# Optimization experiments

Hardware: AMD Instinct MI355X
Metric: run time of the kernel (lower is better)

The kernel has to match this reference:

```python
import jax, jax.numpy as jnp
import numpy as np

# Reconstructed GTS forecasting module (DCGRU encoder-decoder, eval mode / no teacher forcing).
N = 5000        # nodes_num
U = 32          # rnn_units
IN = 1          # node_features per step
K = 2           # max_diffusion_step -> supports [X, A@X, A@A@X]
T_ENC = 12
T_DEC = 12
DIN = (K + 1) * (IN + U)


def setup_inputs() -> dict:
    key = jax.random.key(0)
    ks = jax.random.split(key, 12)
    def p(k, shape, scale=0.1):
        return jax.random.normal(k, shape, dtype=jnp.float32) * scale
    inputs = jax.random.normal(ks[0], (N, T_ENC), dtype=jnp.float32)
    targets = jax.random.normal(ks[1], (N, T_DEC), dtype=jnp.float32)
    adj = jax.random.uniform(ks[2], (N, N), dtype=jnp.float32)
    adj = adj / jnp.sum(adj, axis=1, keepdims=True)  # random-walk normalized support
    return {
        'inputs': inputs, 'targets': targets, 'adj_matrix': adj,
        'enc_Wg': p(ks[3], (DIN, 2 * U)), 'enc_bg': jnp.zeros((2 * U,), jnp.float32),
        'enc_Wc': p(ks[4], (DIN, U)),     'enc_bc': jnp.zeros((U,), jnp.float32),
        'dec_Wg': p(ks[5], (DIN, 2 * U)), 'dec_bg': jnp.zeros((2 * U,), jnp.float32),
        'dec_Wc': p(ks[6], (DIN, U)),     'dec_bc': jnp.zeros((U,), jnp.float32),
        'dec_Wp': p(ks[7], (U, 1)),       'dec_bp': jnp.zeros((1,), jnp.float32),
    }


def _gconv(x, h, adj, W, b):
    # diffusion graph convolution over supports [I, A, A^2]
    xh = jnp.concatenate([x, h], axis=-1)          # [N, IN+U]
    x1 = adj @ xh                                  # [N, IN+U]
    x2 = adj @ x1                                  # [N, IN+U]
    return jnp.concatenate([xh, x1, x2], axis=-1) @ W + b


def _dcgru_step(x, h, adj, Wg, bg, Wc, bc):
    ru = jax.nn.sigmoid(_gconv(x, h, adj, Wg, bg))  # [N, 2U]
    r, u = jnp.split(ru, 2, axis=-1)
    c = jnp.tanh(_gconv(x, r * h, adj, Wc, bc))
    return u * h + (1.0 - u) * c


def reference(inputs, targets, adj_matrix, enc_Wg, enc_bg, enc_Wc, enc_bc,
              dec_Wg, dec_bg, dec_Wc, dec_bc, dec_Wp, dec_bp):
    # ---- encoder: scan DCGRU over encoder_length timesteps ----
    def enc_step(h, xt):  # xt: [N]
        h = _dcgru_step(xt[:, None], h, adj_matrix, enc_Wg, enc_bg, enc_Wc, enc_bc)
        return h, None
    h0 = jnp.zeros((N, U), inputs.dtype)
    h_enc, _ = jax.lax.scan(enc_step, h0, inputs.T)
    go = jnp.zeros((N, 1), inputs.dtype)
    def dec_step(carry, _):
        h, x = carry
        h = _dcgru_step(x, h, adj_matrix, dec_Wg, dec_bg, dec_Wc, dec_bc)
        out = h @ dec_Wp + dec_bp  # [N, 1]
        return (h, out), out
    _, outs = jax.lax.scan(dec_step, (h_enc, go), None, length=T_DEC)
    # torch.cat(outputs, dim=-1) -> [N, T_DEC]
    return outs[:, :, 0].T
```

## Files before the change

kernel.cpp:

```cpp
#include <hip/hip_runtime.h>
#include <type_traits>

constexpr int NN = 5000;
constexpr int NP = 5120;
constexpr int TT = 12;
constexpr int UU = 32;
constexpr int FP = 48;
constexpr int FR = 33;
constexpr int DN = 99;
constexpr int BN = 16;
constexpr int KC = 128;
constexpr int NKC = NP / KC;
constexpr int CPW = NKC / 8;
constexpr int GRID_MM = (NN + BN - 1) / BN;
constexpr int CHE = FP * KC;
constexpr int ACH = BN * KC;

typedef __attribute__((ext_vector_type(8))) short short8;
typedef __attribute__((ext_vector_type(4))) float f32x4;

__device__ __forceinline__ unsigned short f2bf(float x) {
  union { float f; unsigned u; } c; c.f = x;
  return (unsigned short)((c.u + 0x7FFFu + ((c.u >> 16) & 1u)) >> 16);
}

__device__ __forceinline__ int flatXF(int f, int node) {
  int chunk = node >> 7;
  int ks = (node >> 5) & 3;
  int q = (node >> 3) & 3;
  int j = node & 7;
  int t3 = f >> 4;
  int m = f & 15;
  return chunk * CHE + t3 * 2048 + ks * 512 + (m + 16 * q) * 8 + j;
}

__global__ void k_zero(uint4* __restrict__ p, int n) {
  int i = blockIdx.x * 256 + threadIdx.x;
  if (i < n) p[i] = make_uint4(0u, 0u, 0u, 0u);
}

__global__ void k_cast2(const float* __restrict__ adj, unsigned short* __restrict__ adjb) {
  int gid = blockIdx.x * 256 + threadIdx.x;
  int tile = gid >> 8;
  int r2 = gid & 255;
  int nt = tile / NKC, c = tile - nt * NKC;
  int ks = r2 >> 6;
  int qm = r2 & 63;
  int q = qm >> 4, m = qm & 15;
  int n = nt * 16 + m;
  int k = c * 128 + ks * 32 + q * 8;
  union { short8 s; unsigned short u[8]; } o;
  if (n < NN && k < NN) {
    const f32x4* a = reinterpret_cast<const f32x4*>(adj + (size_t)n * NN + k);
    f32x4 x0 = __builtin_nontemporal_load(a);
    f32x4 x1 = __builtin_nontemporal_load(a + 1);
    o.u[0] = f2bf(x0.x); o.u[1] = f2bf(x0.y); o.u[2] = f2bf(x0.z); o.u[3] = f2bf(x0.w);
    o.u[4] = f2bf(x1.x); o.u[5] = f2bf(x1.y); o.u[6] = f2bf(x1.z); o.u[7] = f2bf(x1.w);
  } else {
    o.u[0] = 0; o.u[1] = 0; o.u[2] = 0; o.u[3] = 0;
    o.u[4] = 0; o.u[5] = 0; o.u[6] = 0; o.u[7] = 0;
  }
  *reinterpret_cast<short8*>(adjb + (size_t)gid * 8) = o.s;
}

__global__ void k_initx0(const float* __restrict__ in, float* __restrict__ xf,
                         unsigned short* __restrict__ xb) {
  int n = blockIdx.x * 256 + threadIdx.x;
  if (n >= NP) return;
  float v = (n < NN) ? in[(size_t)n * TT] : 0.f;
  xf[n] = v;
  xb[flatXF(0, n)] = f2bf(v);
}

template <int EPI, bool USEBF>
__global__ __launch_bounds__(512, 4) void k_gemm(
    const unsigned short* __restrict__ adjb, const float* __restrict__ adjf,
    const unsigned short* __restrict__ rhs,
    float* __restrict__ outF, unsigned short* __restrict__ outB,
    const float* __restrict__ s0F, const float* __restrict__ s1F,
    const float* __restrict__ W, const float* __restrict__ bias,
    float* __restrict__ hT, float* __restrict__ uT,
    float* __restrict__ xoF, unsigned short* __restrict__ xoB,
    const float* __restrict__ inp, const float* __restrict__ Wp,
    const float* __restrict__ bp, float* __restrict__ dout,
    int mode, int tnext, int dstep) {
  constexpr int WC = (EPI == 1) ? 64 : 32;
  __shared__ float Pv[8 * FP * BN];
  __shared__ float x2s[(EPI > 0) ? FP * 17 : 1];
  __shared__ float Ws[(EPI > 0) ? DN * WC : 1];

  const int tid = threadIdx.x;
  const int wave = tid >> 6;
  const int lane = tid & 63;
  const int m = lane & 15;
  const int q = lane >> 4;
  const int nodeBase = blockIdx.x * BN;
  const int gn = nodeBase + m;
  const size_t ar = (size_t)((gn < NN) ? gn : NN - 1);

  f32x4 acc0 = {}, acc1 = {}, acc2 = {};
  short8 aCur[4], aNxt[4];

  auto loadA = [&](int i, short8* b) {
    if constexpr (USEBF) {
      const int ch = wave * CPW + i;
      const unsigned short* a0 =
          adjb + ((size_t)blockIdx.x * NKC + ch) * ACH + lane * 8;
#pragma unroll
      for (int ks = 0; ks < 4; ++ks)
        b[ks] = *reinterpret_cast<const short8*>(a0 + ks * 512);
    } else {
      const int k0 = (wave * CPW + i) * KC;
      const float* a0 = adjf + ar * NN;
#pragma unroll
      for (int ks = 0; ks < 4; ++ks) {
        int kb = k0 + ks * 32 + q * 8;
        union { short8 s; unsigned short u[8]; } p0;
        if (kb + 8 <= NN) {
          float4 x0 = *(const float4*)(a0 + kb);
          float4 x1 = *(const float4*)(a0 + kb + 4);
          p0.u[0] = f2bf(x0.x); p0.u[1] = f2bf(x0.y); p0.u[2] = f2bf(x0.z); p0.u[3] = f2bf(x0.w);
          p0.u[4] = f2bf(x1.x); p0.u[5] = f2bf(x1.y); p0.u[6] = f2bf(x1.z); p0.u[7] = f2bf(x1.w);
        } else {
          for (int j = 0; j < 8; ++j) {
            int k = kb + j;
            p0.u[j] = (k < NN) ? f2bf(a0[k]) : (unsigned short)0;
          }
        }
        b[ks] = p0.s;
      }
    }
  };

  loadA(0, aCur);
#pragma unroll
  for (int i = 0; i < CPW; ++i) {
    const int ch = wave * CPW + i;
    short8 cx[12];
    const unsigned short* xb = rhs + (size_t)ch * CHE + lane * 8;
#pragma unroll
    for (int t3 = 0; t3 < 3; ++t3)
#pragma unroll
      for (int ks = 0; ks < 4; ++ks)
        cx[t3 * 4 + ks] = *(const short8*)(xb + t3 * 2048 + ks * 512);
    if (i + 1 < CPW) loadA(i + 1, aNxt);
#pragma unroll
    for (int ks = 0; ks < 4; ++ks) {
      acc0 = __builtin_amdgcn_mfma_f32_16x16x32_bf16(cx[ks], aCur[ks], acc0, 0, 0, 0);
      acc1 = __builtin_amdgcn_mfma_f32_16x16x32_bf16(cx[4 + ks], aCur[ks], acc1, 0, 0, 0);
      acc2 = __builtin_amdgcn_mfma_f32_16x16x32_bf16(cx[8 + ks], aCur[ks], acc2, 0, 0, 0);
    }
#pragma unroll
    for (int ks = 0; ks < 4; ++ks) aCur[ks] = aNxt[ks];
  }

  if constexpr (EPI > 0) {
    for (int i = tid; i < DN * WC; i += 512) Ws[i] = W[i];
  }

#pragma unroll
  for (int r = 0; r < 4; ++r) {
    Pv[wave * (FP * BN) + (q * 4 + r) * BN + m] = acc0[r];
    Pv[wave * (FP * BN) + (16 + q * 4 + r) * BN + m] = acc1[r];
    Pv[wave * (FP * BN) + (32 + q * 4 + r) * BN + m] = acc2[r];
  }
  __syncthreads();

  if constexpr (EPI == 0) {
    for (int e = tid; e < FP * BN; e += 512) {
      int f = e >> 4, n = e & 15;
      float v = 0.f;
#pragma unroll
      for (int w = 0; w < 8; ++w) v += Pv[w * (FP * BN) + e];
      int gn2 = nodeBase + n;
      if (gn2 >= NN) v = 0.f;
      outF[(size_t)f * NP + gn2] = v;
      outB[flatXF(f, gn2)] = f2bf(v);
    }
  } else {
    for (int e = tid; e < FP * BN; e += 512) {
      int f = e >> 4, n = e & 15;
      float v = 0.f;
#pragma unroll
      for (int w = 0; w < 8; ++w) v += Pv[w * (FP * BN) + e];
      x2s[f * 17 + n] = v;
    }
    __syncthreads();
    const int nl = tid & 15;
    const int cg = tid >> 4;
    const int gn2 = nodeBase + nl;
    const bool valid = gn2 < NN;
    const int gnc = valid ? gn2 : NN - 1;
    if constexpr (EPI == 1) {
      float a0 = bias[cg], a1 = bias[cg + 32];
      for (int f = 0; f < FR; ++f) {
        float fe = s0F[(size_t)f * NP + gnc];
        a0 += fe * Ws[f * WC + cg]; a1 += fe * Ws[f * WC + cg + 32];
      }
      for (int f = 0; f < FR; ++f) {
        float fe = s1F[(size_t)f * NP + gnc];
        a0 += fe * Ws[(FR + f) * WC + cg]; a1 += fe * Ws[(FR + f) * WC + cg + 32];
      }
      for (int f = 0; f < FR; ++f) {
        float fe = x2s[f * 17 + nl];
        a0 += fe * Ws[(2 * FR + f) * WC + cg]; a1 += fe * Ws[(2 * FR + f) * WC + cg + 32];
      }
      float r = 1.f / (1.f + expf(-a0));
      float hv = hT[(size_t)cg * NP + gnc];
      float xc = valid ? r * hv : 0.f;
      xoF[(size_t)(1 + cg) * NP + gn2] = xc;
      xoB[flatXF(1 + cg, gn2)] = f2bf(xc);
      float u = 1.f / (1.f + expf(-a1));
      uT[(size_t)cg * NP + gn2] = valid ? u : 0.f;
      if (tid < BN) {
        int g3 = nodeBase + tid;
        float v0 = s0F[g3];
        xoF[g3] = v0;
        xoB[flatXF(0, g3)] = f2bf(v0);
      }
    } else {
      float a0 = bias[cg];
      for (int f = 0; f < FR; ++f) a0 += s0F[(size_t)f * NP + gnc] * Ws[f * WC + cg];
      for (int f = 0; f < FR; ++f) a0 += s1F[(size_t)f * NP + gnc] * Ws[(FR + f) * WC + cg];
      for (int f = 0; f < FR; ++f) a0 += x2s[f * 17 + nl] * Ws[(2 * FR + f) * WC + cg];
      float c = tanhf(a0);
      float u = uT[(size_t)cg * NP + gnc];
      float h0 = hT[(size_t)cg * NP + gnc];
      float hn = u * h0 + (1.f - u) * c;
      float hw = valid ? hn : 0.f;
      hT[(size_t)cg * NP + gn2] = hw;
      xoF[(size_t)(1 + cg) * NP + gn2] = hw;
      xoB[flatXF(1 + cg, gn2)] = f2bf(hw);
      __syncthreads();
      x2s[cg * 17 + nl] = hw;
      __syncthreads();
      if (tid < BN) {
        int g3 = nodeBase + tid;
        bool v3 = g3 < NN;
        float x0 = 0.f;
        if (mode == 0) {
          x0 = v3 ? inp[(size_t)g3 * TT + tnext] : 0.f;
        } else if (mode == 2) {
          float p = bp[0];
          for (int j = 0; j < UU; ++j) p += x2s[j * 17 + tid] * Wp[j];
          if (v3) dout[(size_t)g3 * TT + dstep] = p;
          x0 = v3 ? p : 0.f;
        }
        xoF[g3] = x0;
        xoB[flatXF(0, g3)] = f2bf(x0);
      }
    }
  }
}

extern "C" void kernel_launch(void* const* d_in, const int* in_sizes, int n_in,
                              void* d_out, int out_size, void* d_ws, size_t ws_size,
                              hipStream_t stream) {
  const float* inputs = (const float*)d_in[0];
  const float* adj = (const float*)d_in[2];
  const float* eWg = (const float*)d_in[3];
  const float* eBg = (const float*)d_in[4];
  const float* eWc = (const float*)d_in[5];
  const float* eBc = (const float*)d_in[6];
  const float* dWg = (const float*)d_in[7];
  const float* dBg = (const float*)d_in[8];
  const float* dWc = (const float*)d_in[9];
  const float* dBc = (const float*)d_in[10];
  const float* Wp = (const float*)d_in[11];
  const float* bp = (const float*)d_in[12];
  float* dout = (float*)d_out;

  char* ws = (char*)d_ws;
  size_t o = 0;
  float* xhGf = (float*)(ws + o); o += (size_t)FP * NP * 4;
  unsigned short* xhGb = (unsigned short*)(ws + o); o += (size_t)FP * NP * 2;
  float* xhCf = (float*)(ws + o); o += (size_t)FP * NP * 4;
  unsigned short* xhCb = (unsigned short*)(ws + o); o += (size_t)FP * NP * 2;
  float* x1f = (float*)(ws + o); o += (size_t)FP * NP * 4;
  unsigned short* x1b = (unsigned short*)(ws + o); o += (size_t)FP * NP * 2;
  float* hT = (float*)(ws + o); o += (size_t)UU * NP * 4;
  float* uT = (float*)(ws + o); o += (size_t)UU * NP * 4;
  size_t small = o;
  unsigned short* adjb = (unsigned short*)(ws + o);
  size_t need = o + (size_t)NP * NP * 2;
  bool usebf = ws_size >= need;

  k_zero<<<(int)((small / 16 + 255) / 256), 256, 0, stream>>>((uint4*)ws, (int)(small / 16));
  if (usebf) k_cast2<<<(NP / 8) * NP / 256, 256, 0, stream>>>(adj, adjb);
  k_initx0<<<NP / 256, 256, 0, stream>>>(inputs, xhGf, xhGb);

  auto run = [&](auto ubc) {
    constexpr bool UB = decltype(ubc)::value;
    const unsigned short* ab = UB ? adjb : nullptr;
    for (int t = 0; t < 2 * TT; ++t) {
      bool enc = t < TT;
      const float* Wg = enc ? eWg : dWg;
      const float* Bg = enc ? eBg : dBg;
      const float* Wc = enc ? eWc : dWc;
      const float* Bc = enc ? eBc : dBc;
      int mode, tn = 0, ds = 0;
      if (t < TT - 1) { mode = 0; tn = t + 1; }
      else if (t == TT - 1) { mode = 1; }
      else { mode = 2; ds = t - TT; }

      k_gemm<0, UB><<<GRID_MM, 512, 0, stream>>>(
          ab, adj, xhGb, x1f, x1b,
          nullptr, nullptr, nullptr, nullptr, nullptr, nullptr,
          nullptr, nullptr, nullptr, nullptr, nullptr, nullptr, 0, 0, 0);
      k_gemm<1, UB><<<GRID_MM, 512, 0, stream>>>(
          ab, adj, x1b, nullptr, nullptr,
          xhGf, x1f, Wg, Bg, hT, uT, xhCf, xhCb,
          nullptr, nullptr, nullptr, nullptr, 0, 0, 0);
      k_gemm<0, UB><<<GRID_MM, 512, 0, stream>>>(
          ab, adj, xhCb, x1f, x1b,
          nullptr, nullptr, nullptr, nullptr, nullptr, nullptr,
          nullptr, nullptr, nullptr, nullptr, nullptr, nullptr, 0, 0, 0);
      k_gemm<2, UB><<<GRID_MM, 512, 0, stream>>>(
          ab, adj, x1b, nullptr, nullptr,
          xhCf, x1f, Wc, Bc, hT, uT, xhGf, xhGb,
          inputs, Wp, bp, dout, mode, tn, ds);
    }
  };
  if (usebf) run(std::integral_constant<bool, true>{});
  else run(std::integral_constant<bool, false>{});
}
```

Before: 1.980 ms.

## Process 32 nodes per block to reuse RHS chunk loads across two tiles

Each block now covers 32 destination nodes as two 16-node halves, so every loaded RHS (feature) chunk feeds six MFMAs instead of three. This halves how often the feature operand is re-read from memory across the grid and halves the grid size. Shared memory is merged into one buffer, with the weight staging aliased over the partial-sum area behind an extra barrier, and launch bounds drop to 2 blocks per CU. The costs are higher register pressure and fewer blocks for latency hiding.

```diff
diff --git a/kernel.cpp b/kernel.cpp
--- a/kernel.cpp
+++ b/kernel.cpp
@@ -9,12 +9,14 @@
 constexpr int FR = 33;
 constexpr int DN = 99;
 constexpr int BN = 16;
+constexpr int BNODE = 32;
 constexpr int KC = 128;
 constexpr int NKC = NP / KC;
 constexpr int CPW = NKC / 8;
-constexpr int GRID_MM = (NN + BN - 1) / BN;
+constexpr int GRID_MM = (NN + BNODE - 1) / BNODE;
 constexpr int CHE = FP * KC;
 constexpr int ACH = BN * KC;
+constexpr int PB = FP * BNODE;
 
 typedef __attribute__((ext_vector_type(8))) short short8;
 typedef __attribute__((ext_vector_type(4))) float f32x4;
@@ -73,7 +75,7 @@
 }
 
 template <int EPI, bool USEBF>
-__global__ __launch_bounds__(512, 4) void k_gemm(
+__global__ __launch_bounds__(512, 2) void k_gemm(
     const unsigned short* __restrict__ adjb, const float* __restrict__ adjf,
     const unsigned short* __restrict__ rhs,
     float* __restrict__ outF, unsigned short* __restrict__ outB,
@@ -85,49 +87,55 @@
     const float* __restrict__ bp, float* __restrict__ dout,
     int mode, int tnext, int dstep) {
   constexpr int WC = (EPI == 1) ? 64 : 32;
-  __shared__ float Pv[8 * FP * BN];
-  __shared__ float x2s[(EPI > 0) ? FP * 17 : 1];
-  __shared__ float Ws[(EPI > 0) ? DN * WC : 1];
+  __shared__ float smemF[PB * 8 + FP * 33];
+  float* Pv = smemF;
+  float* x2s = smemF + PB * 8;
+  float* Ws = smemF;
 
   const int tid = threadIdx.x;
   const int wave = tid >> 6;
   const int lane = tid & 63;
   const int m = lane & 15;
   const int q = lane >> 4;
-  const int nodeBase = blockIdx.x * BN;
-  const int gn = nodeBase + m;
-  const size_t ar = (size_t)((gn < NN) ? gn : NN - 1);
-
-  f32x4 acc0 = {}, acc1 = {}, acc2 = {};
-  short8 aCur[4], aNxt[4];
-
-  auto loadA = [&](int i, short8* b) {
+  const int nodeBase = blockIdx.x * BNODE;
+
+  f32x4 acc[2][3] = {};
+  short8 aCur[2][4], aNxt[2][4];
+
+  auto loadA = [&](int i, short8 (&b)[2][4]) {
     if constexpr (USEBF) {
       const int ch = wave * CPW + i;
-      const unsigned short* a0 =
-          adjb + ((size_t)blockIdx.x * NKC + ch) * ACH + lane * 8;
-#pragma unroll
-      for (int ks = 0; ks < 4; ++ks)
-        b[ks] = *reinterpret_cast<const short8*>(a0 + ks * 512);
+#pragma unroll
+      for (int h = 0; h < 2; ++h) {
+        const unsigned short* a0 =
+            adjb + ((size_t)(2 * blockIdx.x + h) * NKC + ch) * ACH + lane * 8;
+#pragma unroll
+        for (int ks = 0; ks < 4; ++ks)
+          b[h][ks] = *reinterpret_cast<const short8*>(a0 + ks * 512);
+      }
     } else {
       const int k0 = (wave * CPW + i) * KC;
-      const float* a0 = adjf + ar * NN;
-#pragma unroll
-      for (int ks = 0; ks < 4; ++ks) {
-        int kb = k0 + ks * 32 + q * 8;
-        union { short8 s; unsigned short u[8]; } p0;
-        if (kb + 8 <= NN) {
-          float4 x0 = *(const float4*)(a0 + kb);
-          float4 x1 = *(const float4*)(a0 + kb + 4);
-          p0.u[0] = f2bf(x0.x); p0.u[1] = f2bf(x0.y); p0.u[2] = f2bf(x0.z); p0.u[3] = f2bf(x0.w);
-          p0.u[4] = f2bf(x1.x); p0.u[5] = f2bf(x1.y); p0.u[6] = f2bf(x1.z); p0.u[7] = f2bf(x1.w);
-        } else {
-          for (int j = 0; j < 8; ++j) {
-            int k = kb + j;
-            p0.u[j] = (k < NN) ? f2bf(a0[k]) : (unsigned short)0;
+#pragma unroll
+      for (int h = 0; h < 2; ++h) {
+        int gnh = nodeBase + h * 16 + m;
+        const float* a0 = adjf + (size_t)((gnh < NN) ? gnh : NN - 1) * NN;
+#pragma unroll
+        for (int ks = 0; ks < 4; ++ks) {
+          int kb = k0 + ks * 32 + q * 8;
+          union { short8 s; unsigned short u[8]; } p0;
+          if (kb + 8 <= NN) {
+            float4 x0 = *(const float4*)(a0 + kb);
+            float4 x1 = *(const float4*)(a0 + kb + 4);
+            p0.u[0] = f2bf(x0.x); p0.u[1] = f2bf(x0.y); p0.u[2] = f2bf(x0.z); p0.u[3] = f2bf(x0.w);
+            p0.u[4] = f2bf(x1.x); p0.u[5] = f2bf(x1.y); p0.u[6] = f2bf(x1.z); p0.u[7] = f2bf(x1.w);
+          } else {
+            for (int j = 0; j < 8; ++j) {
+              int k = kb + j;
+              p0.u[j] = (k < NN) ? f2bf(a0[k]) : (unsigned short)0;
+            }
           }
-        }
-        b[ks] = p0.s;
+          b[h][ks] = p0.s;
+        }
       }
     }
   };
@@ -146,95 +154,109 @@
     if (i + 1 < CPW) loadA(i + 1, aNxt);
 #pragma unroll
     for (int ks = 0; ks < 4; ++ks) {
-      acc0 = __builtin_amdgcn_mfma_f32_16x16x32_bf16(cx[ks], aCur[ks], acc0, 0, 0, 0);
-      acc1 = __builtin_amdgcn_mfma_f32_16x16x32_bf16(cx[4 + ks], aCur[ks], acc1, 0, 0, 0);
-      acc2 = __builtin_amdgcn_mfma_f32_16x16x32_bf16(cx[8 + ks], aCur[ks], acc2, 0, 0, 0);
-    }
-#pragma unroll
-    for (int ks = 0; ks < 4; ++ks) aCur[ks] = aNxt[ks];
+#pragma unroll
+      for (int h = 0; h < 2; ++h) {
+        acc[h][0] = __builtin_amdgcn_mfma_f32_16x16x32_bf16(cx[ks], aCur[h][ks], acc[h][0], 0, 0, 0);
+        acc[h][1] = __builtin_amdgcn_mfma_f32_16x16x32_bf16(cx[4 + ks], aCur[h][ks], acc[h][1], 0, 0, 0);
+        acc[h][2] = __builtin_amdgcn_mfma_f32_16x16x32_bf16(cx[8 + ks], aCur[h][ks], acc[h][2], 0, 0, 0);
+      }
+    }
+#pragma unroll
+    for (int h = 0; h < 2; ++h)
+#pragma unroll
+      for (int ks = 0; ks < 4; ++ks) aCur[h][ks] = aNxt[h][ks];
   }
 
-  if constexpr (EPI > 0) {
-    for (int i = tid; i < DN * WC; i += 512) Ws[i] = W[i];
-  }
-
-#pragma unroll
-  for (int r = 0; r < 4; ++r) {
-    Pv[wave * (FP * BN) + (q * 4 + r) * BN + m] = acc0[r];
-    Pv[wave * (FP * BN) + (16 + q * 4 + r) * BN + m] = acc1[r];
-    Pv[wave * (FP * BN) + (32 + q * 4 + r) * BN + m] = acc2[r];
-  }
+#pragma unroll
+  for (int h = 0; h < 2; ++h)
+#pragma unroll
+    for (int t3 = 0; t3 < 3; ++t3)
+#pragma unroll
+      for (int r = 0; r < 4; ++r)
+        Pv[wave * PB + (t3 * 16 + q * 4 + r) * BNODE + h * 16 + m] = acc[h][t3][r];
   __syncthreads();
 
   if constexpr (EPI == 0) {
-    for (int e = tid; e < FP * BN; e += 512) {
-      int f = e >> 4, n = e & 15;
+    for (int e = tid; e < PB; e += 512) {
+      int f = e >> 5, n = e & 31;
       float v = 0.f;
 #pragma unroll
-      for (int w = 0; w < 8; ++w) v += Pv[w * (FP * BN) + e];
+      for (int w = 0; w < 8; ++w) v += Pv[w * PB + e];
       int gn2 = nodeBase + n;
       if (gn2 >= NN) v = 0.f;
       outF[(size_t)f * NP + gn2] = v;
       outB[flatXF(f, gn2)] = f2bf(v);
     }
   } else {
-    for (int e = tid; e < FP * BN; e += 512) {
-      int f = e >> 4, n = e & 15;
+    for (int e = tid; e < PB; e += 512) {
+      int f = e >> 5, n = e & 31;
       float v = 0.f;
 #pragma unroll
-      for (int w = 0; w < 8; ++w) v += Pv[w * (FP * BN) + e];
-      x2s[f * 17 + n] = v;
-    }
+      for (int w = 0; w < 8; ++w) v += Pv[w * PB + e];
+      x2s[f * 33 + n] = v;
+    }
+    __syncthreads();
+    for (int i = tid; i < DN * WC; i += 512) Ws[i] = W[i];
     __syncthreads();
     const int nl = tid & 15;
     const int cg = tid >> 4;
-    const int gn2 = nodeBase + nl;
-    const bool valid = gn2 < NN;
-    const int gnc = valid ? gn2 : NN - 1;
+    float hwv[2];
+#pragma unroll
+    for (int nh = 0; nh < 2; ++nh) {
+      const int nl2 = nh * 16 + nl;
+      const int gn2 = nodeBase + nl2;
+      const bool valid = gn2 < NN;
+      const int gnc = valid ? gn2 : NN - 1;
+      if constexpr (EPI == 1) {
+        float a0 = bias[cg], a1 = bias[cg + 32];
+        for (int f = 0; f < FR; ++f) {
+          float fe = s0F[(size_t)f * NP + gnc];
+          a0 += fe * Ws[f * WC + cg]; a1 += fe * Ws[f * WC + cg + 32];
+        }
+        for (int f = 0; f < FR; ++f) {
+          float fe = s1F[(size_t)f * NP + gnc];
+          a0 += fe * Ws[(FR + f) * WC + cg]; a1 += fe * Ws[(FR + f) * WC + cg + 32];
+        }
+        for (int f = 0; f < FR; ++f) {
+          float fe = x2s[f * 33 + nl2];
+          a0 += fe * Ws[(2 * FR + f) * WC + cg]; a1 += fe * Ws[(2 * FR + f) * WC + cg + 32];
+        }
+        float r = 1.f / (1.f + expf(-a0));
+        float hv = hT[(size_t)cg * NP + gnc];
+        float xc = valid ? r * hv : 0.f;
+        xoF[(size_t)(1 + cg) * NP + gn2] = xc;
+        xoB[flatXF(1 + cg, gn2)] = f2bf(xc);
+        float u = 1.f / (1.f + expf(-a1));
+        uT[(size_t)cg * NP + gn2] = valid ? u : 0.f;
+      } else {
+        float a0 = bias[cg];
+        for (int f = 0; f < FR; ++f) a0 += s0F[(size_t)f * NP + gnc] * Ws[f * WC + cg];
+        for (int f = 0; f < FR; ++f) a0 += s1F[(size_t)f * NP + gnc] * Ws[(FR + f) * WC + cg];
+        for (int f = 0; f < FR; ++f) a0 += x2s[f * 33 + nl2] * Ws[(2 * FR + f) * WC + cg];
+        float c = tanhf(a0);
+        float u = uT[(size_t)cg * NP + gnc];
+        float h0 = hT[(size_t)cg * NP + gnc];
+        float hn = u * h0 + (1.f - u) * c;
+        float hw = valid ? hn : 0.f;
+        hwv[nh] = hw;
+        hT[(size_t)cg * NP + gn2] = hw;
+        xoF[(size_t)(1 + cg) * NP + gn2] = hw;
+        xoB[flatXF(1 + cg, gn2)] = f2bf(hw);
+      }
+    }
     if constexpr (EPI == 1) {
-      float a0 = bias[cg], a1 = bias[cg + 32];
-      for (int f = 0; f < FR; ++f) {
-        float fe = s0F[(size_t)f * NP + gnc];
-        a0 += fe * Ws[f * WC + cg]; a1 += fe * Ws[f * WC + cg + 32];
-      }
-      for (int f = 0; f < FR; ++f) {
-        float fe = s1F[(size_t)f * NP + gnc];
-        a0 += fe * Ws[(FR + f) * WC + cg]; a1 += fe * Ws[(FR + f) * WC + cg + 32];
-      }
-      for (int f = 0; f < FR; ++f) {
-        float fe = x2s[f * 17 + nl];
-        a0 += fe * Ws[(2 * FR + f) * WC + cg]; a1 += fe * Ws[(2 * FR + f) * WC + cg + 32];
-      }
-      float r = 1.f / (1.f + expf(-a0));
-      float hv = hT[(size_t)cg * NP + gnc];
-      float xc = valid ? r * hv : 0.f;
-      xoF[(size_t)(1 + cg) * NP + gn2] = xc;
-      xoB[flatXF(1 + cg, gn2)] = f2bf(xc);
-      float u = 1.f / (1.f + expf(-a1));
-      uT[(size_t)cg * NP + gn2] = valid ? u : 0.f;
-      if (tid < BN) {
+      if (tid < BNODE) {
         int g3 = nodeBase + tid;
         float v0 = s0F[g3];
         xoF[g3] = v0;
         xoB[flatXF(0, g3)] = f2bf(v0);
       }
     } else {
-      float a0 = bias[cg];
-      for (int f = 0; f < FR; ++f) a0 += s0F[(size_t)f * NP + gnc] * Ws[f * WC + cg];
-      for (int f = 0; f < FR; ++f) a0 += s1F[(size_t)f * NP + gnc] * Ws[(FR + f) * WC + cg];
-      for (int f = 0; f < FR; ++f) a0 += x2s[f * 17 + nl] * Ws[(2 * FR + f) * WC + cg];
-      float c = tanhf(a0);
-      float u = uT[(size_t)cg * NP + gnc];
-      float h0 = hT[(size_t)cg * NP + gnc];
-      float hn = u * h0 + (1.f - u) * c;
-      float hw = valid ? hn : 0.f;
-      hT[(size_t)cg * NP + gn2] = hw;
-      xoF[(size_t)(1 + cg) * NP + gn2] = hw;
-      xoB[flatXF(1 + cg, gn2)] = f2bf(hw);
       __syncthreads();
-      x2s[cg * 17 + nl] = hw;
+      x2s[cg * 33 + nl] = hwv[0];
+      x2s[cg * 33 + 16 + nl] = hwv[1];
       __syncthreads();
-      if (tid < BN) {
+      if (tid < BNODE) {
         int g3 = nodeBase + tid;
         bool v3 = g3 < NN;
         float x0 = 0.f;
@@ -242,7 +264,7 @@
           x0 = v3 ? inp[(size_t)g3 * TT + tnext] : 0.f;
         } else if (mode == 2) {
           float p = bp[0];
-          for (int j = 0; j < UU; ++j) p += x2s[j * 17 + tid] * Wp[j];
+          for (int j = 0; j < UU; ++j) p += x2s[j * 33 + tid] * Wp[j];
           if (v3) dout[(size_t)g3 * TT + dstep] = p;
           x0 = v3 ? p : 0.f;
         }
```

After: 1.796 ms (median of 2 runs). 1.1x faster.
